# Kernel optimization log

Measured on AMD Instinct MI355X. Metric: run time of the kernel, lower is better.

The kernel has to match this reference:

```python
import jax, jax.numpy as jnp
import numpy as np

NUM_EMBEDDINGS = 8192
EMBEDDING_DIM = 512
COMMITMENT_COST = 0.25
EMA_DECAY = 0.99
EPS = 1e-5


def setup_inputs() -> dict:
    key = jax.random.key(0)
    k1, k2, k3, k4 = jax.random.split(key, 4)
    B = 32768
    z = jax.random.normal(k1, (B, EMBEDDING_DIM), dtype=jnp.float32)
    weight = jax.random.normal(k2, (NUM_EMBEDDINGS, EMBEDDING_DIM), dtype=jnp.float32)
    ema_cluster_size = jax.random.uniform(k3, (NUM_EMBEDDINGS,), dtype=jnp.float32)
    ema_dw = jax.random.normal(k4, (NUM_EMBEDDINGS, EMBEDDING_DIM), dtype=jnp.float32)
    return {"z": z, "weight": weight, "ema_cluster_size": ema_cluster_size, "ema_dw": ema_dw}


def reference(z, weight, ema_cluster_size, ema_dw):
    K = weight.shape[0]
    # Squared-L2 distances: (B, K) = |z|^2 + |e|^2 - 2 z e^T
    distances = (
        jnp.sum(z * z, axis=1, keepdims=True)
        + jnp.sum(weight * weight, axis=1)
        - 2.0 * (z @ weight.T)
    )
    indices = jnp.argmin(distances, axis=1)          # (B,)
    quantized_raw = weight[indices]                  # (B, D) gather

    # EMA codebook update (training-mode buffers; one-hot scatter-add == segment_sum)
    counts = jax.ops.segment_sum(jnp.ones(z.shape[0], dtype=z.dtype), indices, num_segments=K)
    dw = jax.ops.segment_sum(z, indices, num_segments=K)  # encodings.T @ z
    new_cluster_size = ema_cluster_size * EMA_DECAY + (1.0 - EMA_DECAY) * counts
    new_ema_dw = ema_dw * EMA_DECAY + (1.0 - EMA_DECAY) * dw
    n = jnp.sum(new_cluster_size)
    cluster_size = (new_cluster_size + EPS) / (n + K * EPS) * n
    new_weight = new_ema_dw / cluster_size[:, None]

    commitment_loss = COMMITMENT_COST * jnp.mean((z - jax.lax.stop_gradient(quantized_raw)) ** 2)
    quantized = z + jax.lax.stop_gradient(quantized_raw - z)  # straight-through
    return quantized, indices, commitment_loss, new_weight, new_cluster_size, new_ema_dw
```

## Files before the change

### kernel.cpp

```cpp
#include <hip/hip_runtime.h>

#define B_N 32768
#define D_N 512
#define K_N 8192
#define EMA 0.99f
#define ONE_M_EMA 0.01f
#define EPS_ 1e-5f
#define CCOST 0.25f

#define ZP_OFF 295936ull
#define WP_OFF 100959232ull
#define WS_NEED (WP_OFF + 25165824ull)
#define CNT_OFF    295936ull
#define OFFS_OFF   332800ull
#define CURS_OFF   365568ull
#define ROWL_OFF   398336ull
#define LPART_OFF  529408ull

typedef __attribute__((ext_vector_type(8))) short bf16x8;
typedef __attribute__((ext_vector_type(4))) float f32x4;

__global__ __launch_bounds__(256) void prep_kernel(const float* __restrict__ w,
                                                   const float* __restrict__ ecs,
                                                   float* __restrict__ wsq,
                                                   float* __restrict__ ncs_out) {
  int row  = blockIdx.x * 4 + (threadIdx.x >> 6);
  int lane = threadIdx.x & 63;
  const float* p = w + (size_t)row * D_N + lane * 8;
  float4 a = *(const float4*)p;
  float4 b = *(const float4*)(p + 4);
  float s = a.x*a.x + a.y*a.y + a.z*a.z + a.w*a.w
          + b.x*b.x + b.y*b.y + b.z*b.z + b.w*b.w;
  #pragma unroll
  for (int off = 32; off; off >>= 1) s += __shfl_down(s, off);
  if (lane == 0) wsq[row] = s;

  int gid = blockIdx.x * 256 + threadIdx.x;
  if (gid < K_N) ncs_out[gid] = EMA * ecs[gid];
}

__global__ __launch_bounds__(256) void prep_nedw(const float4* __restrict__ edw,
                                                 float4* __restrict__ nedw) {
  int i = blockIdx.x * 256 + threadIdx.x;
  float4 v = edw[i];
  v.x *= EMA; v.y *= EMA; v.z *= EMA; v.w *= EMA;
  nedw[i] = v;
}

__global__ __launch_bounds__(256) void split_pack(const float* __restrict__ x,
                                                  ushort* __restrict__ xp,
                                                  int mode) {
  int g   = blockIdx.x * 256 + threadIdx.x;
  int row = g >> 6, c = g & 63;
  const float* src = x + (size_t)row * 512 + c * 8;
  float v[8];
  *(float4*)&v[0] = *(const float4*)&src[0];
  *(float4*)&v[4] = *(const float4*)&src[4];
  uint hw[4], lw[4];
  #pragma unroll
  for (int i = 0; i < 4; i++) {
    uint b0 = __float_as_uint(v[2*i]);
    uint b1 = __float_as_uint(v[2*i+1]);
    float r0 = v[2*i]   - __uint_as_float(b0 & 0xFFFF0000u);
    float r1 = v[2*i+1] - __uint_as_float(b1 & 0xFFFF0000u);
    hw[i] = (b0 >> 16) | (b1 & 0xFFFF0000u);
    lw[i] = (__float_as_uint(r0) >> 16) | (__float_as_uint(r1) & 0xFFFF0000u);
  }
  uint4 H = {hw[0], hw[1], hw[2], hw[3]};
  uint4 L = {lw[0], lw[1], lw[2], lw[3]};
  size_t rb = (size_t)row * 1536;
  int ksl_in = c >> 3;
  int sw = ((c & 7) ^ (row & 7)) * 8;
  size_t d0 = rb + (size_t)(0 * 8 + ksl_in) * 64 + sw;
  size_t d1 = rb + (size_t)(1 * 8 + ksl_in) * 64 + sw;
  size_t d2 = rb + (size_t)(2 * 8 + ksl_in) * 64 + sw;
  if (mode == 0) {
    *(uint4*)&xp[d0] = H; *(uint4*)&xp[d1] = H; *(uint4*)&xp[d2] = L;
  } else {
    *(uint4*)&xp[d0] = H; *(uint4*)&xp[d1] = L; *(uint4*)&xp[d2] = H;
  }
}

constexpr int KSPLIT = 8, COLT = K_N / KSPLIT / 128;

__global__ __launch_bounds__(256, 2) void score3(
    const ushort* __restrict__ zp, const ushort* __restrict__ wp,
    const float* __restrict__ wsq, unsigned long long* __restrict__ packed) {
  __shared__ ushort As[2][128 * 64];
  __shared__ ushort Bs[2][128 * 64];

  const int t = threadIdx.x, lane = t & 63, wid = t >> 6;
  const int wm = wid >> 1, wn = wid & 1;
  const int l15 = lane & 15, lg = lane >> 4;
  const int row0 = blockIdx.x * 128;
  const int ks0  = blockIdx.y * (K_N / KSPLIT);

  const int srow   = wid * 8 + (lane >> 3);
  const int schunk = lane & 7;
  const char* zsb = (const char*)zp + (size_t)(row0 + srow) * 3072 + schunk * 16;

  const int xm = l15 & 7;
  int aoff[4][2], boff[4][2];
  #pragma unroll
  for (int i = 0; i < 4; i++)
    #pragma unroll
    for (int kk = 0; kk < 2; kk++) {
      aoff[i][kk] = (wm * 64 + i * 16 + l15) * 64 + (((kk * 4 + lg) ^ xm) * 8);
      boff[i][kk] = (wn * 64 + i * 16 + l15) * 64 + (((kk * 4 + lg) ^ xm) * 8);
    }

  float rmin[16]; int ridx[16];
  #pragma unroll
  for (int e = 0; e < 16; e++) { rmin[e] = 3.4e38f; ridx[e] = 0; }

  for (int ct = 0; ct < COLT; ct++) {
    const int c0 = ks0 + ct * 128;
    const char* wsb = (const char*)wp + (size_t)(c0 + srow) * 3072 + schunk * 16;

    f32x4 acc[4][4];
    #pragma unroll
    for (int i = 0; i < 4; i++)
      #pragma unroll
      for (int j = 0; j < 4; j++) acc[i][j] = (f32x4){0.f, 0.f, 0.f, 0.f};

    #pragma unroll
    for (int q = 0; q < 4; q++) {
      __builtin_amdgcn_global_load_lds((const unsigned int*)(zsb + q * 98304),
                                       (unsigned int*)&As[0][q * 2048 + wid * 512], 16, 0, 0);
      __builtin_amdgcn_global_load_lds((const unsigned int*)(wsb + q * 98304),
                                       (unsigned int*)&Bs[0][q * 2048 + wid * 512], 16, 0, 0);
    }
    __syncthreads();

    for (int s = 0; s < 24; s++) {
      const int cur = s & 1;
      if (s < 23) {
        const int nxt = cur ^ 1;
        const size_t so = (size_t)(s + 1) * 128;
        #pragma unroll
        for (int q = 0; q < 4; q++) {
          __builtin_amdgcn_global_load_lds((const unsigned int*)(zsb + q * 98304 + so),
                                           (unsigned int*)&As[nxt][q * 2048 + wid * 512], 16, 0, 0);
          __builtin_amdgcn_global_load_lds((const unsigned int*)(wsb + q * 98304 + so),
                                           (unsigned int*)&Bs[nxt][q * 2048 + wid * 512], 16, 0, 0);
        }
      }
      #pragma unroll
      for (int kk = 0; kk < 2; kk++) {
        bf16x8 a[4], b[4];
        #pragma unroll
        for (int i = 0; i < 4; i++) {
          a[i] = *(const bf16x8*)&As[cur][aoff[i][kk]];
          b[i] = *(const bf16x8*)&Bs[cur][boff[i][kk]];
        }
        #pragma unroll
        for (int i = 0; i < 4; i++)
          #pragma unroll
          for (int j = 0; j < 4; j++)
            acc[i][j] = __builtin_amdgcn_mfma_f32_16x16x32_bf16(a[i], b[j], acc[i][j], 0, 0, 0);
      }
      __syncthreads();
    }

    float wq[4];
    #pragma unroll
    for (int j = 0; j < 4; j++) wq[j] = wsq[c0 + wn * 64 + j * 16 + l15];
    #pragma unroll
    for (int i = 0; i < 4; i++)
      #pragma unroll
      for (int r = 0; r < 4; r++) {
        const int e = i * 4 + r;
        #pragma unroll
        for (int j = 0; j < 4; j++) {
          float dist = wq[j] - 2.0f * acc[i][j][r];
          if (dist < rmin[e]) { rmin[e] = dist; ridx[e] = c0 + wn * 64 + j * 16 + l15; }
        }
      }
  }

  #pragma unroll
  for (int e = 0; e < 16; e++) {
    float v = rmin[e]; int ix = ridx[e];
    #pragma unroll
    for (int m = 1; m < 16; m <<= 1) {
      float ov = __shfl_xor(v, m, 64);
      int   oi = __shfl_xor(ix, m, 64);
      if (ov < v || (ov == v && oi < ix)) { v = ov; ix = oi; }
    }
    rmin[e] = v; ridx[e] = ix;
  }
  const int s = l15;
  float bv = 0.f; int bi = 0;
  #pragma unroll
  for (int e = 0; e < 16; e++) {
    bool p = (e == s);
    bv = p ? rmin[e] : bv;
    bi = p ? ridx[e] : bi;
  }
  unsigned u = __float_as_uint(bv);
  u = (u & 0x80000000u) ? ~u : (u | 0x80000000u);
  unsigned long long key = ((unsigned long long)u << 32) | (unsigned)bi;
  atomicMin(&packed[row0 + wm * 64 + (s >> 2) * 16 + lg * 4 + (s & 3)], key);
}

constexpr int LDP = 40;
__device__ __forceinline__ void stage16(const float* __restrict__ g,
                                        ushort* __restrict__ h,
                                        ushort* __restrict__ l) {
  float v[16];
  *(float4*)&v[0]  = *(const float4*)&g[0];
  *(float4*)&v[4]  = *(const float4*)&g[4];
  *(float4*)&v[8]  = *(const float4*)&g[8];
  *(float4*)&v[12] = *(const float4*)&g[12];
  uint hw[8], lw[8];
  #pragma unroll
  for (int i = 0; i < 8; i++) {
    uint b0 = __float_as_uint(v[2*i]);
    uint b1 = __float_as_uint(v[2*i+1]);
    float r0 = v[2*i]   - __uint_as_float(b0 & 0xFFFF0000u);
    float r1 = v[2*i+1] - __uint_as_float(b1 & 0xFFFF0000u);
    hw[i] = (b0 >> 16) | (b1 & 0xFFFF0000u);
    lw[i] = (__float_as_uint(r0) >> 16) | (__float_as_uint(r1) & 0xFFFF0000u);
  }
  ((uint4*)h)[0] = *(uint4*)&hw[0];
  ((uint4*)h)[1] = *(uint4*)&hw[4];
  ((uint4*)l)[0] = *(uint4*)&lw[0];
  ((uint4*)l)[1] = *(uint4*)&lw[4];
}

__global__ __launch_bounds__(256, 2) void score_argmin_mfma(
    const float* __restrict__ z, const float* __restrict__ w,
    const float* __restrict__ wsq, unsigned long long* __restrict__ packed) {
  __shared__ ushort Ah[128][LDP];
  __shared__ ushort Al[128][LDP];
  __shared__ ushort Bh[128][LDP];
  __shared__ ushort Bl[128][LDP];
  const int t = threadIdx.x, lane = t & 63, wid = t >> 6;
  const int wm = wid >> 1, wn = wid & 1;
  const int l15 = lane & 15, lg = lane >> 4;
  const int row0 = blockIdx.x * 128;
  const int ks0  = blockIdx.y * (K_N / KSPLIT);
  const int srow = t >> 1, skq = (t & 1) * 16;
  float rmin[16]; int ridx[16];
  #pragma unroll
  for (int e = 0; e < 16; e++) { rmin[e] = 3.4e38f; ridx[e] = 0; }
  for (int ct = 0; ct < COLT; ct++) {
    const int c0 = ks0 + ct * 128;
    f32x4 acc[4][4];
    #pragma unroll
    for (int i = 0; i < 4; i++)
      #pragma unroll
      for (int j = 0; j < 4; j++) acc[i][j] = (f32x4){0.f, 0.f, 0.f, 0.f};
    for (int k0 = 0; k0 < D_N; k0 += 32) {
      __syncthreads();
      stage16(&z[(size_t)(row0 + srow) * D_N + k0 + skq], &Ah[srow][skq], &Al[srow][skq]);
      stage16(&w[(size_t)(c0   + srow) * D_N + k0 + skq], &Bh[srow][skq], &Bl[srow][skq]);
      __syncthreads();
      bf16x8 ah[4], al[4], bh[4], bl[4];
      #pragma unroll
      for (int i = 0; i < 4; i++) {
        ah[i] = *(const bf16x8*)&Ah[wm*64 + i*16 + l15][lg*8];
        al[i] = *(const bf16x8*)&Al[wm*64 + i*16 + l15][lg*8];
        bh[i] = *(const bf16x8*)&Bh[wn*64 + i*16 + l15][lg*8];
        bl[i] = *(const bf16x8*)&Bl[wn*64 + i*16 + l15][lg*8];
      }
      #pragma unroll
      for (int i = 0; i < 4; i++)
        #pragma unroll
        for (int j = 0; j < 4; j++) {
          acc[i][j] = __builtin_amdgcn_mfma_f32_16x16x32_bf16(ah[i], bh[j], acc[i][j], 0, 0, 0);
          acc[i][j] = __builtin_amdgcn_mfma_f32_16x16x32_bf16(ah[i], bl[j], acc[i][j], 0, 0, 0);
          acc[i][j] = __builtin_amdgcn_mfma_f32_16x16x32_bf16(al[i], bh[j], acc[i][j], 0, 0, 0);
        }
    }
    float wq[4];
    #pragma unroll
    for (int j = 0; j < 4; j++) wq[j] = wsq[c0 + wn*64 + j*16 + l15];
    #pragma unroll
    for (int i = 0; i < 4; i++)
      #pragma unroll
      for (int r = 0; r < 4; r++) {
        const int e = i * 4 + r;
        #pragma unroll
        for (int j = 0; j < 4; j++) {
          float dist = wq[j] - 2.0f * acc[i][j][r];
          if (dist < rmin[e]) { rmin[e] = dist; ridx[e] = c0 + wn*64 + j*16 + l15; }
        }
      }
  }
  #pragma unroll
  for (int e = 0; e < 16; e++) {
    float v = rmin[e]; int ix = ridx[e];
    #pragma unroll
    for (int m = 1; m < 16; m <<= 1) {
      float ov = __shfl_xor(v, m, 64);
      int   oi = __shfl_xor(ix, m, 64);
      if (ov < v || (ov == v && oi < ix)) { v = ov; ix = oi; }
    }
    rmin[e] = v; ridx[e] = ix;
  }
  const int s = l15;
  float bv = 0.f; int bi = 0;
  #pragma unroll
  for (int e = 0; e < 16; e++) {
    bool p = (e == s);
    bv = p ? rmin[e] : bv;
    bi = p ? ridx[e] : bi;
  }
  unsigned u = __float_as_uint(bv);
  u = (u & 0x80000000u) ? ~u : (u | 0x80000000u);
  unsigned long long key = ((unsigned long long)u << 32) | (unsigned)bi;
  atomicMin(&packed[row0 + wm*64 + (s >> 2)*16 + lg*4 + (s & 3)], key);
}

__global__ __launch_bounds__(256) void count_kernel(
    const unsigned long long* __restrict__ packed, int* __restrict__ cnt,
    float* __restrict__ idxout) {
  int row = blockIdx.x * 256 + threadIdx.x;
  int idx = (int)(packed[row] & 0xFFFFFFFFull);
  idxout[row] = (float)idx;
  atomicAdd(&cnt[idx], 1);
}

__global__ __launch_bounds__(256) void scan_kernel(const int* __restrict__ cnt,
                                                   int* __restrict__ offs,
                                                   int* __restrict__ cursor) {
  int t = threadIdx.x;
  int base = t * 32;
  int local[32];
  int s = 0;
  #pragma unroll
  for (int i = 0; i < 32; i++) { local[i] = s; s += cnt[base + i]; }
  __shared__ int ps[257];
  ps[t + 1] = s;
  if (t == 0) ps[0] = 0;
  __syncthreads();
  if (t == 0) { for (int i = 1; i <= 256; i++) ps[i] += ps[i - 1]; }
  __syncthreads();
  int e = ps[t];
  #pragma unroll
  for (int i = 0; i < 32; i++) {
    int o = e + local[i];
    offs[base + i] = o; cursor[base + i] = o;
  }
  if (t == 255) offs[8192] = ps[256];
}

__global__ __launch_bounds__(256) void scatter_ids(
    const unsigned long long* __restrict__ packed, int* __restrict__ cursor,
    int* __restrict__ rowlist) {
  int row = blockIdx.x * 256 + threadIdx.x;
  int idx = (int)(packed[row] & 0xFFFFFFFFull);
  int pos = atomicAdd(&cursor[idx], 1);
  rowlist[pos] = row;
}

__global__ __launch_bounds__(256) void seg_accum(
    const float* __restrict__ z, const float* __restrict__ edw,
    const float* __restrict__ ecs, const int* __restrict__ offs,
    const int* __restrict__ rowlist, float* __restrict__ nedw_out,
    float* __restrict__ ncs_out) {
  int k = blockIdx.x, t = threadIdx.x;
  int s0 = offs[k], s1 = offs[k + 1];
  float ax = 0.f, ay = 0.f;
  for (int r = s0; r < s1; r++) {
    int row = rowlist[r];
    float2 zv = *(const float2*)&z[(size_t)row * D_N + t * 2];
    ax += zv.x; ay += zv.y;
  }
  float2 ev = *(const float2*)&edw[(size_t)k * D_N + t * 2];
  float2 o;
  o.x = EMA * ev.x + ONE_M_EMA * ax;
  o.y = EMA * ev.y + ONE_M_EMA * ay;
  *(float2*)&nedw_out[(size_t)k * D_N + t * 2] = o;
  if (t == 0) ncs_out[k] = EMA * ecs[k] + ONE_M_EMA * (float)(s1 - s0);
}

__global__ __launch_bounds__(256) void quant_loss(
    const float* __restrict__ z, const float* __restrict__ w,
    const unsigned long long* __restrict__ packed,
    float* __restrict__ qout, float* __restrict__ lpart) {
  int row = blockIdx.x, t = threadIdx.x;
  int idx = (int)(packed[row] & 0xFFFFFFFFull);
  float2 zv = *(const float2*)&z[(size_t)row * D_N + t * 2];
  float2 wv = *(const float2*)&w[(size_t)idx * D_N + t * 2];
  float2 q;
  q.x = zv.x + (wv.x - zv.x);
  q.y = zv.y + (wv.y - zv.y);
  *(float2*)&qout[(size_t)row * D_N + t * 2] = q;
  float dx = zv.x - wv.x, dy = zv.y - wv.y;
  float s = dx * dx + dy * dy;
  #pragma unroll
  for (int off = 32; off; off >>= 1) s += __shfl_down(s, off);
  __shared__ float part[4];
  if ((t & 63) == 0) part[t >> 6] = s;
  __syncthreads();
  if (t == 0) lpart[row] = part[0] + part[1] + part[2] + part[3];
}

__global__ __launch_bounds__(256) void reduce2(const float* __restrict__ ncs_out,
                                               const float* __restrict__ lpart,
                                               float* __restrict__ nsum,
                                               float* __restrict__ loss_sum) {
  int t = threadIdx.x;
  float s1 = 0.f, s2 = 0.f;
  for (int i = t; i < K_N; i += 256) s1 += ncs_out[i];
  for (int i = t; i < B_N; i += 256) s2 += lpart[i];
  #pragma unroll
  for (int off = 32; off; off >>= 1) {
    s1 += __shfl_down(s1, off);
    s2 += __shfl_down(s2, off);
  }
  __shared__ float p1[4], p2[4];
  if ((t & 63) == 0) { p1[t >> 6] = s1; p2[t >> 6] = s2; }
  __syncthreads();
  if (t == 0) {
    nsum[0]     = p1[0] + p1[1] + p1[2] + p1[3];
    loss_sum[0] = p2[0] + p2[1] + p2[2] + p2[3];
  }
}

__global__ __launch_bounds__(256) void gather_scatter(
    const float* __restrict__ z, const float* __restrict__ w,
    const unsigned long long* __restrict__ packed,
    float* __restrict__ qout, float* __restrict__ idxout,
    float* __restrict__ ncs_out, float* __restrict__ nedw_out,
    float* __restrict__ loss_sum) {
  int row = blockIdx.x;
  int t   = threadIdx.x;
  int idx = (int)(packed[row] & 0xFFFFFFFFull);
  float2 zv = *(const float2*)&z[(size_t)row * D_N + t * 2];
  float2 wv = *(const float2*)&w[(size_t)idx * D_N + t * 2];
  float2 q;
  q.x = zv.x + (wv.x - zv.x);
  q.y = zv.y + (wv.y - zv.y);
  *(float2*)&qout[(size_t)row * D_N + t * 2] = q;
  float dx = zv.x - wv.x, dy = zv.y - wv.y;
  float s = dx*dx + dy*dy;
  #pragma unroll
  for (int off = 32; off; off >>= 1) s += __shfl_down(s, off);
  __shared__ float part[4];
  if ((t & 63) == 0) part[t >> 6] = s;
  __syncthreads();
  if (t == 0) {
    atomicAdd(loss_sum, part[0] + part[1] + part[2] + part[3]);
    atomicAdd(&ncs_out[idx], ONE_M_EMA);
    idxout[row] = (float)idx;
  }
  atomicAdd(&nedw_out[(size_t)idx * D_N + t*2],     ONE_M_EMA * zv.x);
  atomicAdd(&nedw_out[(size_t)idx * D_N + t*2 + 1], ONE_M_EMA * zv.y);
}

__global__ __launch_bounds__(256) void reduce_n(const float* __restrict__ ncs_out,
                                                float* __restrict__ nsum) {
  int t = threadIdx.x;
  float s = 0.f;
  for (int i = t; i < K_N; i += 256) s += ncs_out[i];
  #pragma unroll
  for (int off = 32; off; off >>= 1) s += __shfl_down(s, off);
  __shared__ float part[4];
  if ((t & 63) == 0) part[t >> 6] = s;
  __syncthreads();
  if (t == 0) nsum[0] = part[0] + part[1] + part[2] + part[3];
}

__global__ __launch_bounds__(256) void finalize(
    const float* __restrict__ ncs_out, const float* __restrict__ nedw_out,
    float* __restrict__ nw_out, const float* __restrict__ nsum,
    const float* __restrict__ loss_sum, float* __restrict__ loss_out) {
  size_t i = (size_t)blockIdx.x * 256 + threadIdx.x;
  float n = nsum[0];
  int k = (int)(i >> 9);
  float nv = ncs_out[k];
  float cs = (nv + EPS_) / (n + K_N * EPS_) * n;
  nw_out[i] = nedw_out[i] / cs;
  if (i == 0) loss_out[0] = CCOST * loss_sum[0] / (float)((size_t)B_N * D_N);
}

extern "C" void kernel_launch(void* const* d_in, const int* in_sizes, int n_in,
                              void* d_out, int out_size, void* d_ws, size_t ws_size,
                              hipStream_t stream) {
  const float* z   = (const float*)d_in[0];
  const float* w   = (const float*)d_in[1];
  const float* ecs = (const float*)d_in[2];
  const float* edw = (const float*)d_in[3];

  float* out      = (float*)d_out;
  float* qout     = out;
  float* idxout   = out + (size_t)B_N * D_N;
  float* loss_out = idxout + B_N;
  float* nw_out   = loss_out + 1;
  float* ncs_out  = nw_out + (size_t)K_N * D_N;
  float* nedw_out = ncs_out + K_N;

  unsigned long long* packed = (unsigned long long*)d_ws;
  float* wsq      = (float*)((char*)d_ws + 262144);
  float* loss_sum = (float*)((char*)d_ws + 294912);
  float* nsum     = loss_sum + 1;

  hipMemsetAsync(d_ws, 0xFF, 262144, stream);
  hipMemsetAsync((void*)loss_sum, 0, 8, stream);

  prep_kernel<<<2048, 256, 0, stream>>>(w, ecs, wsq, ncs_out);

  if (ws_size >= WS_NEED) {
    ushort* zp  = (ushort*)((char*)d_ws + ZP_OFF);
    ushort* wp  = (ushort*)((char*)d_ws + WP_OFF);
    int* cnt    = (int*)((char*)d_ws + CNT_OFF);
    int* offs   = (int*)((char*)d_ws + OFFS_OFF);
    int* cursor = (int*)((char*)d_ws + CURS_OFF);
    int* rowl   = (int*)((char*)d_ws + ROWL_OFF);
    float* lpart= (float*)((char*)d_ws + LPART_OFF);

    split_pack<<<8192, 256, 0, stream>>>(z, zp, 0);
    split_pack<<<2048, 256, 0, stream>>>(w, wp, 1);
    score3<<<dim3(B_N / 128, KSPLIT), 256, 0, stream>>>(zp, wp, wsq, packed);
    hipMemsetAsync((void*)cnt, 0, K_N * sizeof(int), stream);
    count_kernel<<<B_N / 256, 256, 0, stream>>>(packed, cnt, idxout);
    scan_kernel<<<1, 256, 0, stream>>>(cnt, offs, cursor);
    scatter_ids<<<B_N / 256, 256, 0, stream>>>(packed, cursor, rowl);
    seg_accum<<<K_N, 256, 0, stream>>>(z, edw, ecs, offs, rowl, nedw_out, ncs_out);
    quant_loss<<<B_N, 256, 0, stream>>>(z, w, packed, qout, lpart);
    reduce2<<<1, 256, 0, stream>>>(ncs_out, lpart, nsum, loss_sum);
  } else {
    prep_nedw<<<4096, 256, 0, stream>>>((const float4*)edw, (float4*)nedw_out);
    score_argmin_mfma<<<dim3(B_N / 128, KSPLIT), 256, 0, stream>>>(z, w, wsq, packed);
    gather_scatter<<<B_N, 256, 0, stream>>>(z, w, packed, qout, idxout,
                                            ncs_out, nedw_out, loss_sum);
    reduce_n<<<1, 256, 0, stream>>>(ncs_out, nsum);
  }

  finalize<<<K_N * D_N / 256, 256, 0, stream>>>(ncs_out, nedw_out, nw_out,
                                                nsum, loss_sum, loss_out);
}
```

Measured before the change: 1.148 ms.

## Restructure split-bf16 distance GEMM into 256x256 tiles with 4-stage continuous pipeline

Changes the packed bf16 hi/lo layout of z and the codebook from row-major per-row slabs to k-slice-major planes, so each 16-wide k step is a contiguous block. The scoring kernel now uses 512 threads with 256x256 output tiles per column step, a 4-deep LDS ring buffer that prefetches across column tiles, explicit vmcnt waits and raw barriers. The per-row argmin is reduced in shared memory before a single atomicMin per row. The goal is to raise MFMA arithmetic intensity and hide global-load latency. In exchange it uses much more LDS and more registers (32 accumulators per lane), which could lower occupancy or cause spills, and the hand-written waitcnt logic is fragile.

Result: slower. 1.304 ms (+13.6%).

```diff
diff --git a/kernel.cpp b/kernel.cpp
--- a/kernel.cpp
+++ b/kernel.cpp
@@ -49,7 +49,7 @@
 
 __global__ __launch_bounds__(256) void split_pack(const float* __restrict__ x,
                                                   ushort* __restrict__ xp,
-                                                  int mode) {
+                                                  int R, int mode) {
   int g   = blockIdx.x * 256 + threadIdx.x;
   int row = g >> 6, c = g & 63;
   const float* src = x + (size_t)row * 512 + c * 8;
@@ -68,142 +68,150 @@
   }
   uint4 H = {hw[0], hw[1], hw[2], hw[3]};
   uint4 L = {lw[0], lw[1], lw[2], lw[3]};
-  size_t rb = (size_t)row * 1536;
-  int ksl_in = c >> 3;
-  int sw = ((c & 7) ^ (row & 7)) * 8;
-  size_t d0 = rb + (size_t)(0 * 8 + ksl_in) * 64 + sw;
-  size_t d1 = rb + (size_t)(1 * 8 + ksl_in) * 64 + sw;
-  size_t d2 = rb + (size_t)(2 * 8 + ksl_in) * 64 + sw;
-  if (mode == 0) {
-    *(uint4*)&xp[d0] = H; *(uint4*)&xp[d1] = H; *(uint4*)&xp[d2] = L;
-  } else {
-    *(uint4*)&xp[d0] = H; *(uint4*)&xp[d1] = L; *(uint4*)&xp[d2] = H;
-  }
-}
-
-constexpr int KSPLIT = 8, COLT = K_N / KSPLIT / 128;
-
-__global__ __launch_bounds__(256, 2) void score3(
+  int si  = c >> 2;
+  int p   = (c & 3) ^ ((row >> 1) & 3);
+  size_t sstr = (size_t)R * 32;
+  size_t base = (size_t)row * 32 + (size_t)p * 8;
+  size_t d0 = (size_t)(si)      * sstr + base;
+  size_t d1 = (size_t)(16 + si) * sstr + base;
+  size_t d2 = (size_t)(32 + si) * sstr + base;
+  if (mode == 0) { *(uint4*)&xp[d0] = H; *(uint4*)&xp[d1] = H; *(uint4*)&xp[d2] = L; }
+  else           { *(uint4*)&xp[d0] = H; *(uint4*)&xp[d1] = L; *(uint4*)&xp[d2] = H; }
+}
+
+constexpr int COLT2 = 8;
+
+#define GLDS(SRC, DST) __builtin_amdgcn_global_load_lds((const unsigned int*)(SRC), (unsigned int*)(DST), 16, 0, 0)
+
+__global__ __launch_bounds__(512, 2) void score3p(
     const ushort* __restrict__ zp, const ushort* __restrict__ wp,
     const float* __restrict__ wsq, unsigned long long* __restrict__ packed) {
-  __shared__ ushort As[2][128 * 64];
-  __shared__ ushort Bs[2][128 * 64];
+  __shared__ ushort As[4][8192];
+  __shared__ ushort Bs[4][8192];
+  __shared__ float wsqs[2048];
+  __shared__ unsigned long long best2[256][4];
 
   const int t = threadIdx.x, lane = t & 63, wid = t >> 6;
-  const int wm = wid >> 1, wn = wid & 1;
-  const int l15 = lane & 15, lg = lane >> 4;
-  const int row0 = blockIdx.x * 128;
-  const int ks0  = blockIdx.y * (K_N / KSPLIT);
-
-  const int srow   = wid * 8 + (lane >> 3);
-  const int schunk = lane & 7;
-  const char* zsb = (const char*)zp + (size_t)(row0 + srow) * 3072 + schunk * 16;
-
-  const int xm = l15 & 7;
-  int aoff[4][2], boff[4][2];
-  #pragma unroll
-  for (int i = 0; i < 4; i++)
-    #pragma unroll
-    for (int kk = 0; kk < 2; kk++) {
-      aoff[i][kk] = (wm * 64 + i * 16 + l15) * 64 + (((kk * 4 + lg) ^ xm) * 8);
-      boff[i][kk] = (wn * 64 + i * 16 + l15) * 64 + (((kk * 4 + lg) ^ xm) * 8);
+  const int wm = wid >> 2, wn = wid & 3;
+  const int l15 = lane & 15, lg = (lane >> 4) & 3;
+  const int row0 = blockIdx.x * 256;
+  const int cg0  = blockIdx.y * 2048;
+
+  const char* zA = (const char*)zp + ((size_t)(row0 + (t >> 2)) * 64 + (size_t)(t & 3) * 16);
+  const char* wB = (const char*)wp + ((size_t)(cg0  + (t >> 2)) * 64 + (size_t)(t & 3) * 16);
+
+  const int swz  = (l15 >> 1) & 3;
+  const int aoff = (wm * 128 + l15) * 64 + ((lg ^ swz) * 16);
+  const int boff = (wn * 64  + l15) * 64 + ((lg ^ swz) * 16);
+
+  { float4 v = *(const float4*)&wsq[cg0 + t * 4]; *(float4*)&wsqs[t * 4] = v; }
+  if (t < 256) { best2[t][0] = ~0ull; best2[t][1] = ~0ull; best2[t][2] = ~0ull; best2[t][3] = ~0ull; }
+  #pragma unroll
+  for (int s0 = 0; s0 < 3; s0++) {
+    GLDS(zA + (size_t)s0 * 2097152,        (char*)As[s0] + t * 16);
+    GLDS(zA + (size_t)s0 * 2097152 + 8192, (char*)As[s0] + 8192 + t * 16);
+    GLDS(wB + (size_t)s0 * 524288,         (char*)Bs[s0] + t * 16);
+    GLDS(wB + (size_t)s0 * 524288 + 8192,  (char*)Bs[s0] + 8192 + t * 16);
+  }
+  __syncthreads();
+
+  int sf = 3, ctf = 0;
+  for (int ct = 0; ct < COLT2; ct++) {
+    f32x4 acc[8][4];
+    #pragma unroll
+    for (int i = 0; i < 8; i++)
+      #pragma unroll
+      for (int j = 0; j < 4; j++) acc[i][j] = (f32x4){0.f, 0.f, 0.f, 0.f};
+
+    for (int s = 0; s < 48; s++) {
+      const int slot = s & 3;
+      if (ctf < COLT2) {
+        const int slotF = sf & 3;
+        GLDS(zA + (size_t)sf * 2097152,        (char*)As[slotF] + t * 16);
+        GLDS(zA + (size_t)sf * 2097152 + 8192, (char*)As[slotF] + 8192 + t * 16);
+        const size_t wOfs = (size_t)sf * 524288 + (size_t)ctf * 16384;
+        GLDS(wB + wOfs,        (char*)Bs[slotF] + t * 16);
+        GLDS(wB + wOfs + 8192, (char*)Bs[slotF] + 8192 + t * 16);
+        sf++; if (sf == 48) { sf = 0; ctf++; }
+      }
+      bf16x8 a[8], b[4];
+      const char* Ab = (const char*)As[slot] + aoff;
+      const char* Bb = (const char*)Bs[slot] + boff;
+      #pragma unroll
+      for (int i = 0; i < 8; i++) a[i] = *(const bf16x8*)(Ab + i * 1024);
+      #pragma unroll
+      for (int j = 0; j < 4; j++) b[j] = *(const bf16x8*)(Bb + j * 1024);
+      __builtin_amdgcn_s_setprio(1);
+      #pragma unroll
+      for (int i = 0; i < 8; i++)
+        #pragma unroll
+        for (int j = 0; j < 4; j++)
+          acc[i][j] = __builtin_amdgcn_mfma_f32_16x16x32_bf16(a[i], b[j], acc[i][j], 0, 0, 0);
+      __builtin_amdgcn_s_setprio(0);
+      const int Sg = ct * 48 + s;
+      if (Sg < COLT2 * 48 - 3)       { asm volatile("s_waitcnt vmcnt(8)" ::: "memory"); }
+      else if (Sg == COLT2 * 48 - 3) { asm volatile("s_waitcnt vmcnt(4)" ::: "memory"); }
+      else if (Sg == COLT2 * 48 - 2) { asm volatile("s_waitcnt vmcnt(0)" ::: "memory"); }
+      __builtin_amdgcn_s_barrier();
+      __builtin_amdgcn_sched_barrier(0);
     }
 
-  float rmin[16]; int ridx[16];
-  #pragma unroll
-  for (int e = 0; e < 16; e++) { rmin[e] = 3.4e38f; ridx[e] = 0; }
-
-  for (int ct = 0; ct < COLT; ct++) {
-    const int c0 = ks0 + ct * 128;
-    const char* wsb = (const char*)wp + (size_t)(c0 + srow) * 3072 + schunk * 16;
-
-    f32x4 acc[4][4];
-    #pragma unroll
-    for (int i = 0; i < 4; i++)
-      #pragma unroll
-      for (int j = 0; j < 4; j++) acc[i][j] = (f32x4){0.f, 0.f, 0.f, 0.f};
-
-    #pragma unroll
-    for (int q = 0; q < 4; q++) {
-      __builtin_amdgcn_global_load_lds((const unsigned int*)(zsb + q * 98304),
-                                       (unsigned int*)&As[0][q * 2048 + wid * 512], 16, 0, 0);
-      __builtin_amdgcn_global_load_lds((const unsigned int*)(wsb + q * 98304),
-                                       (unsigned int*)&Bs[0][q * 2048 + wid * 512], 16, 0, 0);
-    }
-    __syncthreads();
-
-    for (int s = 0; s < 24; s++) {
-      const int cur = s & 1;
-      if (s < 23) {
-        const int nxt = cur ^ 1;
-        const size_t so = (size_t)(s + 1) * 128;
-        #pragma unroll
-        for (int q = 0; q < 4; q++) {
-          __builtin_amdgcn_global_load_lds((const unsigned int*)(zsb + q * 98304 + so),
-                                           (unsigned int*)&As[nxt][q * 2048 + wid * 512], 16, 0, 0);
-          __builtin_amdgcn_global_load_lds((const unsigned int*)(wsb + q * 98304 + so),
-                                           (unsigned int*)&Bs[nxt][q * 2048 + wid * 512], 16, 0, 0);
-        }
-      }
-      #pragma unroll
-      for (int kk = 0; kk < 2; kk++) {
-        bf16x8 a[4], b[4];
-        #pragma unroll
-        for (int i = 0; i < 4; i++) {
-          a[i] = *(const bf16x8*)&As[cur][aoff[i][kk]];
-          b[i] = *(const bf16x8*)&Bs[cur][boff[i][kk]];
-        }
-        #pragma unroll
-        for (int i = 0; i < 4; i++)
-          #pragma unroll
-          for (int j = 0; j < 4; j++)
-            acc[i][j] = __builtin_amdgcn_mfma_f32_16x16x32_bf16(a[i], b[j], acc[i][j], 0, 0, 0);
-      }
-      __syncthreads();
-    }
-
-    float wq[4];
-    #pragma unroll
-    for (int j = 0; j < 4; j++) wq[j] = wsq[c0 + wn * 64 + j * 16 + l15];
-    #pragma unroll
-    for (int i = 0; i < 4; i++)
+    float rv[32]; int rx[32];
+    #pragma unroll
+    for (int i = 0; i < 8; i++)
       #pragma unroll
       for (int r = 0; r < 4; r++) {
-        const int e = i * 4 + r;
+        float bvv = 3.4e38f; int bii = 0;
         #pragma unroll
         for (int j = 0; j < 4; j++) {
-          float dist = wq[j] - 2.0f * acc[i][j][r];
-          if (dist < rmin[e]) { rmin[e] = dist; ridx[e] = c0 + wn * 64 + j * 16 + l15; }
+          float wq = wsqs[ct * 256 + wn * 64 + j * 16 + l15];
+          float dist = wq - 2.0f * acc[i][j][r];
+          int c = cg0 + ct * 256 + wn * 64 + j * 16 + l15;
+          if (dist < bvv) { bvv = dist; bii = c; }
         }
+        rv[i * 4 + r] = bvv; rx[i * 4 + r] = bii;
       }
-  }
-
-  #pragma unroll
-  for (int e = 0; e < 16; e++) {
-    float v = rmin[e]; int ix = ridx[e];
-    #pragma unroll
-    for (int m = 1; m < 16; m <<= 1) {
-      float ov = __shfl_xor(v, m, 64);
-      int   oi = __shfl_xor(ix, m, 64);
-      if (ov < v || (ov == v && oi < ix)) { v = ov; ix = oi; }
+    #pragma unroll
+    for (int e = 0; e < 32; e++) {
+      float v = rv[e]; int ix = rx[e];
+      #pragma unroll
+      for (int m = 1; m < 16; m <<= 1) {
+        float ov = __shfl_xor(v, m, 64);
+        int   oi = __shfl_xor(ix, m, 64);
+        if (ov < v || (ov == v && oi < ix)) { v = ov; ix = oi; }
+      }
+      rv[e] = v; rx[e] = ix;
     }
-    rmin[e] = v; ridx[e] = ix;
-  }
-  const int s = l15;
-  float bv = 0.f; int bi = 0;
-  #pragma unroll
-  for (int e = 0; e < 16; e++) {
-    bool p = (e == s);
-    bv = p ? rmin[e] : bv;
-    bi = p ? ridx[e] : bi;
-  }
-  unsigned u = __float_as_uint(bv);
-  u = (u & 0x80000000u) ? ~u : (u | 0x80000000u);
-  unsigned long long key = ((unsigned long long)u << 32) | (unsigned)bi;
-  atomicMin(&packed[row0 + wm * 64 + (s >> 2) * 16 + lg * 4 + (s & 3)], key);
+    #pragma unroll
+    for (int half = 0; half < 2; half++) {
+      const int e0 = l15 + half * 16;
+      float bvv = 0.f; int bii = 0;
+      #pragma unroll
+      for (int e = 0; e < 32; e++) {
+        bool p = (e == e0);
+        bvv = p ? rv[e] : bvv; bii = p ? rx[e] : bii;
+      }
+      unsigned u = __float_as_uint(bvv);
+      u = (u & 0x80000000u) ? ~u : (u | 0x80000000u);
+      unsigned long long key = ((unsigned long long)u << 32) | (unsigned)bii;
+      const int rowl = wm * 128 + (e0 >> 2) * 16 + lg * 4 + (e0 & 3);
+      unsigned long long cur = best2[rowl][wn];
+      if (key < cur) best2[rowl][wn] = key;
+    }
+  }
+
+  __syncthreads();
+  if (t < 256) {
+    unsigned long long k0 = best2[t][0], k1 = best2[t][1];
+    unsigned long long k2 = best2[t][2], k3 = best2[t][3];
+    unsigned long long m0 = k0 < k1 ? k0 : k1;
+    unsigned long long m1 = k2 < k3 ? k2 : k3;
+    atomicMin(&packed[row0 + t], m0 < m1 ? m0 : m1);
+  }
 }
 
 constexpr int LDP = 40;
+constexpr int KSPLIT = 8, COLT = K_N / KSPLIT / 128;
 __device__ __forceinline__ void stage16(const float* __restrict__ g,
                                         ushort* __restrict__ h,
                                         ushort* __restrict__ l) {
@@ -512,9 +520,9 @@
     int* rowl   = (int*)((char*)d_ws + ROWL_OFF);
     float* lpart= (float*)((char*)d_ws + LPART_OFF);
 
-    split_pack<<<8192, 256, 0, stream>>>(z, zp, 0);
-    split_pack<<<2048, 256, 0, stream>>>(w, wp, 1);
-    score3<<<dim3(B_N / 128, KSPLIT), 256, 0, stream>>>(zp, wp, wsq, packed);
+    split_pack<<<8192, 256, 0, stream>>>(z, zp, B_N, 0);
+    split_pack<<<2048, 256, 0, stream>>>(w, wp, K_N, 1);
+    score3p<<<dim3(128, 4), 512, 0, stream>>>(zp, wp, wsq, packed);
     hipMemsetAsync((void*)cnt, 0, K_N * sizeof(int), stream);
     count_kernel<<<B_N / 256, 256, 0, stream>>>(packed, cnt, idxout);
     scan_kernel<<<1, 256, 0, stream>>>(cnt, offs, cursor);
```
